# Kernel tuning notes

Hardware: AMD Instinct MI355X
Metric: run time of the kernel (lower is better)

The kernel has to match this reference:

```python
import jax, jax.numpy as jnp
import numpy as np

N_NODES = 10000
N_EDGES = 160000
MUL_N = 64    # node-feature multiplicity per irrep (0e and 1o)
MUL_F = 16    # field-feature multiplicity per irrep
SQ3 = np.sqrt(3.0).astype(np.float32)
SILU_GAIN = np.float32(1.679177)  # e3nn normalize2mom gain for silu


def split_irreps(x, mul):
    # x: [n, mul + 3*mul] laid out e3nn-style: scalars then vectors
    return x[:, :mul], x[:, mul:].reshape(x.shape[0], mul, 3)


def irrep_linear(s, v, Ws, Wv):
    # o3.Linear on (mul x0e + mul x1o): per-irrep channel mixing, 1/sqrt(fan_in)
    inv = np.float32(1.0 / np.sqrt(Ws.shape[0]))
    return (s @ Ws) * inv, jnp.einsum('nui,uv->nvi', v, Wv) * inv


def setup_inputs() -> dict:
    key = jax.random.key(0)
    ks = jax.random.split(key, 30)
    f32 = jnp.float32
    rn = lambda k, sh: jax.random.normal(k, sh, dtype=f32)
    inp = {
        'node_attrs': rn(ks[0], (N_NODES, 10)),
        'node_feats': rn(ks[1], (N_NODES, MUL_N + 3 * MUL_N)),
        'edge_attrs': rn(ks[2], (N_EDGES, 4)),
        'edge_feats': rn(ks[3], (N_EDGES, 8)),
        'field_feats': rn(ks[4], (N_NODES, MUL_F + 3 * MUL_F)),
        'edge_index': jax.random.randint(ks[5], (2, N_EDGES), 0, N_NODES, dtype=jnp.int32),
        # o3.Linear weights (linear1, linear2)
        'W1s': rn(ks[6], (MUL_N, MUL_N)), 'W1v': rn(ks[7], (MUL_N, MUL_N)),
        'W2s': rn(ks[8], (MUL_N, MUL_N)), 'W2v': rn(ks[9], (MUL_N, MUL_N)),
        # FullyConnectedNet [8,64,64,64,256]
        'mlp_w1': rn(ks[10], (8, 64)), 'mlp_w2': rn(ks[11], (64, 64)),
        'mlp_w3': rn(ks[12], (64, 64)), 'mlp_w4': rn(ks[13], (64, 4 * MUL_N)),
        # linear_v_sender / linear_v_receiver: 128x0e+128x1o -> 16x0e+16x1o
        'Wvs_s': rn(ks[14], (2 * MUL_N, MUL_F)), 'Wvs_v': rn(ks[15], (2 * MUL_N, MUL_F)),
        'Wvr_s': rn(ks[16], (2 * MUL_N, MUL_F)), 'Wvr_v': rn(ks[17], (2 * MUL_N, MUL_F)),
        # final FC tensor products (field x field -> 1x0e)
        'Wfs0': rn(ks[18], (MUL_F, MUL_F)), 'Wfs1': rn(ks[19], (MUL_F, MUL_F)),
        'Wfr0': rn(ks[20], (MUL_F, MUL_F)), 'Wfr1': rn(ks[21], (MUL_F, MUL_F)),
        # LinearInFieldChargesBlock FC TP: node x field -> 1x0e+1x1o
        'Wmp_ss': rn(ks[22], (MUL_N, MUL_F)), 'Wmp_vv': rn(ks[23], (MUL_N, MUL_F)),
        'Wmp_sv': rn(ks[24], (MUL_N, MUL_F)), 'Wmp_vs': rn(ks[25], (MUL_N, MUL_F)),
    }
    return inp


def reference(node_attrs, node_feats, edge_attrs, edge_feats, field_feats,
              W1s, W1v, W2s, W2v, mlp_w1, mlp_w2, mlp_w3, mlp_w4,
              Wvs_s, Wvs_v, Wvr_s, Wvr_v, Wfs0, Wfs1, Wfr0, Wfr1,
              Wmp_ss, Wmp_vv, Wmp_sv, Wmp_vs, edge_index):
    sender, receiver = edge_index[0], edge_index[1]
    num_nodes = node_feats.shape[0]

    # conv_tp weight MLP (e3nn FullyConnectedNet)
    h = edge_feats
    for W in (mlp_w1, mlp_w2, mlp_w3):
        h = jax.nn.silu((h @ W) * np.float32(1.0 / np.sqrt(W.shape[0]))) * SILU_GAIN
    tp_w = (h @ mlp_w4) * np.float32(1.0 / np.sqrt(mlp_w4.shape[0]))  # [E, 4*MUL_N]
    w = tp_w.reshape(-1, 4, MUL_N)

    ns, nv = split_irreps(node_feats, MUL_N)
    l1s, l1v = irrep_linear(ns, nv, W1s, W1v)
    l2s, l2v = irrep_linear(ns, nv, W2s, W2v)
    bs = l1s[sender] + l2s[receiver]   # [E, MUL_N]
    bv = l1v[sender] + l2v[receiver]   # [E, MUL_N, 3]

    y0 = edge_attrs[:, 0:1]            # [E,1] 0e harmonic
    y1 = edge_attrs[:, 1:4]            # [E,3] 1o harmonic
    # uvu CG tensor product with per-edge weights
    m00 = w[:, 0] * bs * y0                                          # 0e x 0e -> 0e
    m11 = w[:, 1] * jnp.einsum('eui,ei->eu', bv, y1) / SQ3           # 1o x 1o -> 0e
    m01 = w[:, 2][:, :, None] * bs[:, :, None] * y1[:, None, :]      # 0e x 1o -> 1o
    m10 = w[:, 3][:, :, None] * bv * y0[:, :, None]                  # 1o x 0e -> 1o
    ms = jnp.concatenate([m00, m11], axis=1)    # [E, 128]
    mv = jnp.concatenate([m01, m10], axis=1)    # [E, 128, 3]

    As, Av = irrep_linear(ms, mv, Wvs_s, Wvs_v)
    Bs, Bv = irrep_linear(ms, mv, Wvr_s, Wvr_v)

    fs, fv = split_irreps(field_feats, MUL_F)
    alpha = np.float32(1.0 / np.sqrt(2 * MUL_F * MUL_F))
    p_s = (jnp.einsum('eu,ev,uv->e', As, fs[sender], Wfs0)
           + jnp.einsum('eui,evi,uv->e', Av, fv[sender], Wfs1) / SQ3) * alpha
    p_r = (jnp.einsum('eu,ev,uv->e', Bs, fs[receiver], Wfr0)
           + jnp.einsum('eui,evi,uv->e', Bv, fv[receiver], Wfr1) / SQ3) * alpha
    p_ji = np.float32(0.1) * (p_s + p_r)   # [E]

    charges = (jax.ops.segment_sum(p_ji, receiver, num_segments=num_nodes)
               - jax.ops.segment_sum(p_ji, sender, num_segments=num_nodes))

    # field-dependent multipoles (FC TP, zero_charges=True then charge slot overwritten)
    a2 = np.float32(1.0 / np.sqrt(2 * MUL_N * MUL_F))
    mp0 = (jnp.einsum('nu,nv,uv->n', ns, fs, Wmp_ss)
           + jnp.einsum('nui,nvi,uv->n', nv, fv, Wmp_vv) / SQ3) * a2
    mp1 = (jnp.einsum('nu,nvi,uv->ni', ns, fv, Wmp_sv)
           + jnp.einsum('nui,nv,uv->ni', nv, fs, Wmp_vs)) * a2
    mpoles = np.float32(0.01) * jnp.concatenate([mp0[:, None], mp1], axis=1)  # [N,4]
    mpoles = mpoles.at[:, 0].set(charges)
    return mpoles[:, None, :], p_ji[:, None]
```

## Files before the change

### kernel.cpp

```cpp
#include <hip/hip_runtime.h>

#define NN 10000
#define NE 160000

#define INV8   0.35355339059327373f
#define QINV   0.125f
#define GAIN   1.679177f
#define ISQ3   0.57735026918962576f
#define FINALS 4.8828125e-5f
#define MPSC   2.2097086912079612e-4f

typedef __attribute__((ext_vector_type(8))) short bf16x8;
typedef __attribute__((ext_vector_type(4))) float f32x4;

__device__ __forceinline__ float4 ld4(const float* p){ return *(const float4*)p; }
__device__ __forceinline__ float sil(float x){ return x*GAIN/(1.f+__expf(-x)); }
__device__ __forceinline__ unsigned short f2b(float f){
  unsigned u = __float_as_uint(f);
  return (unsigned short)((u + 0x7FFFu + ((u>>16)&1u)) >> 16);
}
__device__ __forceinline__ float b2f(unsigned short b){
  return __uint_as_float(((unsigned)b) << 16);
}
__device__ __forceinline__ void st4b(unsigned short* p, float a, float b, float c, float d){
  unsigned long long v = (unsigned long long)f2b(a)
                       | ((unsigned long long)f2b(b) << 16)
                       | ((unsigned long long)f2b(c) << 32)
                       | ((unsigned long long)f2b(d) << 48);
  *(unsigned long long*)p = v;
}
__device__ __forceinline__ void up8(const unsigned short* p, float* f){
  const uint4 v = *(const uint4*)p;
  f[0]=__uint_as_float(v.x<<16); f[1]=__uint_as_float(v.x&0xFFFF0000u);
  f[2]=__uint_as_float(v.y<<16); f[3]=__uint_as_float(v.y&0xFFFF0000u);
  f[4]=__uint_as_float(v.z<<16); f[5]=__uint_as_float(v.z&0xFFFF0000u);
  f[6]=__uint_as_float(v.w<<16); f[7]=__uint_as_float(v.w&0xFFFF0000u);
}
#define C4(v,i) (((const float*)&(v))[i])

__global__ __launch_bounds__(256) void sort_zero(unsigned* __restrict__ hist){
  hist[blockIdx.x*256 + threadIdx.x] = 0u;
}
__global__ __launch_bounds__(256) void sort_hist(const int* __restrict__ eidx,
                                                 unsigned* __restrict__ hist){
  const int e = blockIdx.x*256 + threadIdx.x;
  atomicAdd(&hist[eidx[NE + e]], 1u);
}
__global__ __launch_bounds__(256) void sort_scan(const unsigned* __restrict__ hist,
                                                 unsigned* __restrict__ offs){
  __shared__ unsigned part[256];
  __shared__ unsigned base[256];
  const int t = threadIdx.x;
  unsigned s = 0;
  #pragma unroll
  for (int i = 0; i < 40; ++i) s += hist[t*40 + i];
  part[t] = s;
  __syncthreads();
  if (t == 0) {
    unsigned run = 0;
    for (int i = 0; i < 256; ++i) { base[i] = run; run += part[i]; }
  }
  __syncthreads();
  unsigned run = base[t];
  #pragma unroll
  for (int i = 0; i < 40; ++i) { offs[t*40 + i] = run; run += hist[t*40 + i]; }
}
__global__ __launch_bounds__(256) void sort_scatter(const int* __restrict__ eidx,
                                                    unsigned* __restrict__ offs,
                                                    unsigned* __restrict__ sorted){
  const int e = blockIdx.x*256 + threadIdx.x;
  const unsigned pos = atomicAdd(&offs[eidx[NE + e]], 1u);
  sorted[pos] = (unsigned)e;
}
__global__ __launch_bounds__(256) void permute_kernel(
    const unsigned* __restrict__ sorted,
    const float* __restrict__ efe, const float* __restrict__ ea,
    const int* __restrict__ eidx,
    float* __restrict__ pefe, float* __restrict__ pea,
    int* __restrict__ psr, int* __restrict__ peid)
{
  const int i = blockIdx.x*256 + threadIdx.x;
  const int e = (int)sorted[i];
  const float4 a = ld4(efe + (size_t)e*8);
  const float4 b = ld4(efe + (size_t)e*8 + 4);
  *(float4*)(pefe + (size_t)i*8)     = a;
  *(float4*)(pefe + (size_t)i*8 + 4) = b;
  *(float4*)(pea  + (size_t)i*4)     = ld4(ea + (size_t)e*4);
  psr[i]      = eidx[e];
  psr[NE + i] = eidx[NE + e];
  peid[i]     = e;
}

#define WQ_STRIDE 260
__global__ __launch_bounds__(256, 2) void edge_fused_kernel(
    const float* __restrict__ efe,
    const float* __restrict__ mw1, const float* __restrict__ mw2,
    const float* __restrict__ mw3, const float* __restrict__ mw4,
    const float* __restrict__ ea, const int* __restrict__ eidx,
    const int* __restrict__ peid,
    const unsigned short* __restrict__ wsS, const unsigned short* __restrict__ wsR,
    float* __restrict__ out)
{
  __shared__ __align__(16) unsigned char pool[8192 + 128*WQ_STRIDE*2];
  unsigned short* W4q = (unsigned short*)pool;
  unsigned short* W1t = (unsigned short*)(pool + 8192);
  unsigned short* W2t = (unsigned short*)(pool + 12288);
  unsigned short* W3t = (unsigned short*)(pool + 20480);
  unsigned short* H   = (unsigned short*)(pool + 28672);
  unsigned short* WQ  = (unsigned short*)(pool + 8192);

  const int tid = threadIdx.x;
  const int wv  = tid >> 6;
  const int l   = tid & 63;
  const int eb  = blockIdx.x * 128;

  #pragma unroll
  for (int it = 0; it < 16; ++it) {
    const int i = tid + 256*it, e = i >> 5, k = i & 31;
    H[e*64 + (k ^ ((e&7)<<3))] = (k < 8) ? f2b(efe[(size_t)(eb+e)*8 + k]) : 0;
  }
  #pragma unroll
  for (int it = 0; it < 8; ++it) {
    const int i = tid + 256*it, n = i >> 5, k = i & 31;
    W1t[n*32 + (k ^ ((n&3)<<3))] = (k < 8) ? f2b(mw1[k*64 + n]) : 0;
  }
  #pragma unroll
  for (int it = 0; it < 16; ++it) {
    const int i = tid + 256*it, k = i >> 6, n = i & 63;
    W2t[n*64 + (k ^ ((n&7)<<3))] = f2b(mw2[k*64 + n]);
    W3t[n*64 + (k ^ ((n&7)<<3))] = f2b(mw3[k*64 + n]);
  }
  __syncthreads();

  const int arow = l & 15;
  const int koff = (l >> 4) * 8;

  {
    bf16x8 a[8];
    #pragma unroll
    for (int mf = 0; mf < 8; ++mf) {
      const int e = mf*16 + arow;
      a[mf] = *(const bf16x8*)&H[e*64 + (koff ^ ((e&7)<<3))];
    }
    const int n = wv*16 + arow;
    const bf16x8 b = *(const bf16x8*)&W1t[n*32 + (koff ^ ((n&3)<<3))];
    __syncthreads();
    f32x4 acc[8];
    #pragma unroll
    for (int mf = 0; mf < 8; ++mf) {
      acc[mf] = (f32x4){0.f,0.f,0.f,0.f};
      acc[mf] = __builtin_amdgcn_mfma_f32_16x16x32_bf16(a[mf], b, acc[mf], 0, 0, 0);
    }
    #pragma unroll
    for (int mf = 0; mf < 8; ++mf)
      #pragma unroll
      for (int rg = 0; rg < 4; ++rg) {
        const int e = mf*16 + (l>>4)*4 + rg, j = wv*16 + arow;
        H[e*64 + (j ^ ((e&7)<<3))] = f2b(sil(acc[mf][rg]*INV8));
      }
    __syncthreads();
  }

  const unsigned short* Wt[2] = { W2t, W3t };
  #pragma unroll
  for (int ly = 0; ly < 2; ++ly) {
    bf16x8 a[16];
    #pragma unroll
    for (int mf = 0; mf < 8; ++mf)
      #pragma unroll
      for (int ks = 0; ks < 2; ++ks) {
        const int e = mf*16 + arow, kb = ks*32 + koff;
        a[mf*2+ks] = *(const bf16x8*)&H[e*64 + (kb ^ ((e&7)<<3))];
      }
    const int n = wv*16 + arow;
    bf16x8 b0, b1;
    {
      const int kb0 = koff, kb1 = 32 + koff;
      b0 = *(const bf16x8*)&Wt[ly][n*64 + (kb0 ^ ((n&7)<<3))];
      b1 = *(const bf16x8*)&Wt[ly][n*64 + (kb1 ^ ((n&7)<<3))];
    }
    __syncthreads();
    f32x4 acc[8];
    #pragma unroll
    for (int mf = 0; mf < 8; ++mf) {
      acc[mf] = (f32x4){0.f,0.f,0.f,0.f};
      acc[mf] = __builtin_amdgcn_mfma_f32_16x16x32_bf16(a[mf*2+0], b0, acc[mf], 0, 0, 0);
      acc[mf] = __builtin_amdgcn_mfma_f32_16x16x32_bf16(a[mf*2+1], b1, acc[mf], 0, 0, 0);
    }
    #pragma unroll
    for (int mf = 0; mf < 8; ++mf)
      #pragma unroll
      for (int rg = 0; rg < 4; ++rg) {
        const int e = mf*16 + (l>>4)*4 + rg, j = wv*16 + arow;
        H[e*64 + (j ^ ((e&7)<<3))] = f2b(sil(acc[mf][rg]*QINV));
      }
    __syncthreads();
  }

  bf16x8 a4[16];
  #pragma unroll
  for (int mf = 0; mf < 8; ++mf)
    #pragma unroll
    for (int ks = 0; ks < 2; ++ks) {
      const int e = mf*16 + arow, kb = ks*32 + koff;
      a4[mf*2+ks] = *(const bf16x8*)&H[e*64 + (kb ^ ((e&7)<<3))];
    }

  for (int q = 0; q < 4; ++q) {
    #pragma unroll
    for (int it = 0; it < 16; ++it) {
      const int i = tid + 256*it, k = i >> 6, nn = i & 63;
      W4q[nn*64 + (k ^ ((nn&7)<<3))] = f2b(mw4[k*256 + q*64 + nn]);
    }
    __syncthreads();

    const int n = wv*16 + arow;
    const bf16x8 b0 = *(const bf16x8*)&W4q[n*64 + ((koff     ) ^ ((n&7)<<3))];
    const bf16x8 b1 = *(const bf16x8*)&W4q[n*64 + ((32 + koff) ^ ((n&7)<<3))];
    f32x4 acc[8];
    #pragma unroll
    for (int mf = 0; mf < 8; ++mf) {
      acc[mf] = (f32x4){0.f,0.f,0.f,0.f};
      acc[mf] = __builtin_amdgcn_mfma_f32_16x16x32_bf16(a4[mf*2+0], b0, acc[mf], 0, 0, 0);
      acc[mf] = __builtin_amdgcn_mfma_f32_16x16x32_bf16(a4[mf*2+1], b1, acc[mf], 0, 0, 0);
    }
    #pragma unroll
    for (int mf = 0; mf < 8; ++mf)
      #pragma unroll
      for (int rg = 0; rg < 4; ++rg) {
        const int e = mf*16 + (l>>4)*4 + rg;
        const int j = q*64 + wv*16 + arow;
        WQ[e*WQ_STRIDE + j] = f2b(acc[mf][rg]);
      }
    __syncthreads();
  }

  {
    const int el  = tid >> 1;
    const int sub = tid & 1;
    const int e   = eb + el;
    const int s = eidx[e];
    const int r = eidx[NE + e];
    const float4 y = ld4(ea + (size_t)e*4);

    float accS = 0.f, accR = 0.f;
    const unsigned short* Sb = wsS + (size_t)s*768 + sub*384;
    const unsigned short* Rb = wsR + (size_t)r*768 + sub*384;
    const unsigned short* wrow = WQ + el*WQ_STRIDE;
    #pragma unroll 2
    for (int t = 0; t < 8; ++t) {
      const int uq = sub*8 + t;
      const unsigned short* Sr = Sb + t*48;
      const unsigned short* Rr = Rb + t*48;
      float S[48], R[48];
      up8(Sr+ 0, S+ 0); up8(Sr+ 8, S+ 8); up8(Sr+16, S+16);
      up8(Sr+24, S+24); up8(Sr+32, S+32); up8(Sr+40, S+40);
      up8(Rr+ 0, R+ 0); up8(Rr+ 8, R+ 8); up8(Rr+16, R+16);
      up8(Rr+24, R+24); up8(Rr+32, R+32); up8(Rr+40, R+40);

      float wq[16];
      #pragma unroll
      for (int m = 0; m < 4; ++m) {
        const unsigned long long v = *(const unsigned long long*)(wrow + m*64 + uq*4);
        #pragma unroll
        for (int d = 0; d < 4; ++d)
          wq[m*4+d] = b2f((unsigned short)(v >> (16*d)));
      }

      #pragma unroll
      for (int d = 0; d < 4; ++d) {
        const float bs = S[d]    + R[d];
        const float b0 = S[4+d]  + R[4+d];
        const float b1 = S[8+d]  + R[8+d];
        const float b2 = S[12+d] + R[12+d];
        const float bvy = b0*y.y + b1*y.z + b2*y.w;
        const float m0 = wq[d]    * bs * y.x;
        const float m1 = wq[4+d]  * bvy;
        const float m2 = wq[8+d]  * bs;
        const float m3 = wq[12+d] * y.x;
        accS += m0*S[16+d] + m1*S[20+d]
              + m2*(y.y*S[24+d] + y.z*S[28+d] + y.w*S[32+d])
              + m3*(b0*S[36+d] + b1*S[40+d] + b2*S[44+d]);
        accR += m0*R[16+d] + m1*R[20+d]
              + m2*(y.y*R[24+d] + y.z*R[28+d] + y.w*R[32+d])
              + m3*(b0*R[36+d] + b1*R[40+d] + b2*R[44+d]);
      }
    }
    float acc = FINALS * (accS + accR);
    acc += __shfl_xor(acc, 1, 64);
    if (sub == 0) {
      out[NN*4 + peid[e]] = acc;
      atomicAdd(out + (size_t)r*4, acc);
      atomicAdd(out + (size_t)s*4, -acc);
    }
  }
}

__global__ __launch_bounds__(256) void node_kernel(
    const float* __restrict__ nf, const float* __restrict__ ff,
    const float* __restrict__ W1s, const float* __restrict__ W1v,
    const float* __restrict__ W2s, const float* __restrict__ W2v,
    const float* __restrict__ Wvss, const float* __restrict__ Wvsv,
    const float* __restrict__ Wvrs, const float* __restrict__ Wvrv,
    const float* __restrict__ Wfs0, const float* __restrict__ Wfs1,
    const float* __restrict__ Wfr0, const float* __restrict__ Wfr1,
    const float* __restrict__ Wmsv, const float* __restrict__ Wmvs,
    unsigned short* __restrict__ wsS, unsigned short* __restrict__ wsR,
    float* __restrict__ out)
{
  const int lane = threadIdx.x & 63;
  const int Wid  = blockIdx.x * 4 + (threadIdx.x >> 6);
  const int p    = __builtin_amdgcn_readfirstlane(Wid & 7);
  const int grp  = __builtin_amdgcn_readfirstlane(Wid >> 3);
  const int n = grp * 64 + lane;
  if (n >= NN) return;
  const float* nrow = nf + (size_t)n * 256;
  const int vb = p * 8;
  const size_t rec = (size_t)n * 768;

  float a1s[8], a2s[8], a1v[3][8], a2v[3][8], t1[16];
  #pragma unroll
  for (int j = 0; j < 8; ++j){ a1s[j]=0.f; a2s[j]=0.f;
    a1v[0][j]=0.f; a1v[1][j]=0.f; a1v[2][j]=0.f;
    a2v[0][j]=0.f; a2v[1][j]=0.f; a2v[2][j]=0.f; }
  #pragma unroll
  for (int j = 0; j < 16; ++j) t1[j]=0.f;

  for (int u = 0; u < 64; ++u) {
    const float su  = nrow[u];
    const float nv0 = nrow[64+u*3+0];
    const float nv1 = nrow[64+u*3+1];
    const float nv2 = nrow[64+u*3+2];
    const float4 s1a = ld4(W1s+u*64+vb), s1b = ld4(W1s+u*64+vb+4);
    const float4 s2a = ld4(W2s+u*64+vb), s2b = ld4(W2s+u*64+vb+4);
    const float4 v1a = ld4(W1v+u*64+vb), v1b = ld4(W1v+u*64+vb+4);
    const float4 v2a = ld4(W2v+u*64+vb), v2b = ld4(W2v+u*64+vb+4);
    #pragma unroll
    for (int d = 0; d < 4; ++d) {
      a1s[d]     += su*C4(s1a,d);  a1s[4+d]     += su*C4(s1b,d);
      a2s[d]     += su*C4(s2a,d);  a2s[4+d]     += su*C4(s2b,d);
      a1v[0][d]  += nv0*C4(v1a,d); a1v[0][4+d]  += nv0*C4(v1b,d);
      a1v[1][d]  += nv1*C4(v1a,d); a1v[1][4+d]  += nv1*C4(v1b,d);
      a1v[2][d]  += nv2*C4(v1a,d); a1v[2][4+d]  += nv2*C4(v1b,d);
      a2v[0][d]  += nv0*C4(v2a,d); a2v[0][4+d]  += nv0*C4(v2b,d);
      a2v[1][d]  += nv1*C4(v2a,d); a2v[1][4+d]  += nv1*C4(v2b,d);
      a2v[2][d]  += nv2*C4(v2a,d); a2v[2][4+d]  += nv2*C4(v2b,d);
    }
    if (p == 0) {
      #pragma unroll
      for (int q = 0; q < 4; ++q) {
        const float4 m = ld4(Wmsv + u*16 + q*4);
        t1[q*4]   += su*m.x; t1[q*4+1] += su*m.y;
        t1[q*4+2] += su*m.z; t1[q*4+3] += su*m.w;
      }
    }
  }
  #pragma unroll
  for (int hh = 0; hh < 2; ++hh) {
    const int uq = 2*p + hh, o = hh*4;
    unsigned short* S = wsS + rec + uq*48;
    unsigned short* R = wsR + rec + uq*48;
    st4b(S+0,  a1s[o]*QINV, a1s[o+1]*QINV, a1s[o+2]*QINV, a1s[o+3]*QINV);
    st4b(S+4,  a1v[0][o]*QINV, a1v[0][o+1]*QINV, a1v[0][o+2]*QINV, a1v[0][o+3]*QINV);
    st4b(S+8,  a1v[1][o]*QINV, a1v[1][o+1]*QINV, a1v[1][o+2]*QINV, a1v[1][o+3]*QINV);
    st4b(S+12, a1v[2][o]*QINV, a1v[2][o+1]*QINV, a1v[2][o+2]*QINV, a1v[2][o+3]*QINV);
    st4b(R+0,  a2s[o]*QINV, a2s[o+1]*QINV, a2s[o+2]*QINV, a2s[o+3]*QINV);
    st4b(R+4,  a2v[0][o]*QINV, a2v[0][o+1]*QINV, a2v[0][o+2]*QINV, a2v[0][o+3]*QINV);
    st4b(R+8,  a2v[1][o]*QINV, a2v[1][o+1]*QINV, a2v[1][o+2]*QINV, a2v[1][o+3]*QINV);
    st4b(R+12, a2v[2][o]*QINV, a2v[2][o+1]*QINV, a2v[2][o+2]*QINV, a2v[2][o+3]*QINV);
  }

  float fsv[16], fvv[48];
  {
    const float* fr = ff + (size_t)n*64;
    #pragma unroll
    for (int q = 0; q < 4; ++q) {
      const float4 t = ld4(fr + q*4);
      fsv[q*4]=t.x; fsv[q*4+1]=t.y; fsv[q*4+2]=t.z; fsv[q*4+3]=t.w;
    }
    #pragma unroll
    for (int q = 0; q < 12; ++q) {
      const float4 t = ld4(fr + 16 + q*4);
      fvv[q*4]=t.x; fvv[q*4+1]=t.y; fvv[q*4+2]=t.z; fvv[q*4+3]=t.w;
    }
  }

  if (p == 0) {
    float m0=0.f, m1=0.f, m2=0.f;
    #pragma unroll
    for (int v = 0; v < 16; ++v) {
      m0 += t1[v]*fvv[v*3]; m1 += t1[v]*fvv[v*3+1]; m2 += t1[v]*fvv[v*3+2];
    }
    for (int u = 0; u < 64; ++u) {
      float t2 = 0.f;
      #pragma unroll
      for (int q = 0; q < 4; ++q) {
        const float4 w = ld4(Wmvs + u*16 + q*4);
        t2 += w.x*fsv[q*4] + w.y*fsv[q*4+1] + w.z*fsv[q*4+2] + w.w*fsv[q*4+3];
      }
      m0 += nrow[64+u*3+0]*t2;
      m1 += nrow[64+u*3+1]*t2;
      m2 += nrow[64+u*3+2]*t2;
    }
    float* o = out + (size_t)n*4;
    o[0] = 0.f;
    o[1] = MPSC*m0; o[2] = MPSC*m1; o[3] = MPSC*m2;
  }

  float gsA[16], gsB[16], gvA[48], gvB[48];
  #pragma unroll
  for (int up = 0; up < 16; ++up) {
    float sA=0.f,sB=0.f,vA0=0.f,vA1=0.f,vA2=0.f,vB0=0.f,vB1=0.f,vB2=0.f;
    #pragma unroll
    for (int q = 0; q < 4; ++q) {
      const float4 w0 = ld4(Wfs0 + up*16 + q*4);
      const float4 w1 = ld4(Wfs1 + up*16 + q*4);
      const float4 w2 = ld4(Wfr0 + up*16 + q*4);
      const float4 w3 = ld4(Wfr1 + up*16 + q*4);
      #pragma unroll
      for (int d = 0; d < 4; ++d) {
        const int v = q*4+d;
        sA  += C4(w0,d)*fsv[v];
        sB  += C4(w2,d)*fsv[v];
        vA0 += C4(w1,d)*fvv[v*3]; vA1 += C4(w1,d)*fvv[v*3+1]; vA2 += C4(w1,d)*fvv[v*3+2];
        vB0 += C4(w3,d)*fvv[v*3]; vB1 += C4(w3,d)*fvv[v*3+1]; vB2 += C4(w3,d)*fvv[v*3+2];
      }
    }
    gsA[up]=sA; gsB[up]=sB;
    gvA[up*3]=vA0; gvA[up*3+1]=vA1; gvA[up*3+2]=vA2;
    gvB[up*3]=vB0; gvB[up*3+1]=vB1; gvB[up*3+2]=vB2;
  }

  #pragma unroll
  for (int tq = 0; tq < 4; ++tq) {
    float qa[4], qb[4], ra[3][4], rb[3][4];
    #pragma unroll
    for (int d = 0; d < 4; ++d) {
      const int U = p*16 + tq*4 + d;
      float aq=0.f,bq=0.f,a0=0.f,a1=0.f,a2=0.f,b0=0.f,b1=0.f,b2=0.f;
      #pragma unroll
      for (int q = 0; q < 4; ++q) {
        const float4 ws_ = ld4(Wvss + U*16 + q*4);
        const float4 wr_ = ld4(Wvrs + U*16 + q*4);
        const float4 wv_ = ld4(Wvsv + U*16 + q*4);
        const float4 wu_ = ld4(Wvrv + U*16 + q*4);
        #pragma unroll
        for (int dd = 0; dd < 4; ++dd) {
          const int up = q*4+dd;
          aq += C4(ws_,dd)*gsA[up];
          bq += C4(wr_,dd)*gsB[up];
          a0 += C4(wv_,dd)*gvA[up*3]; a1 += C4(wv_,dd)*gvA[up*3+1]; a2 += C4(wv_,dd)*gvA[up*3+2];
          b0 += C4(wu_,dd)*gvB[up*3]; b1 += C4(wu_,dd)*gvB[up*3+1]; b2 += C4(wu_,dd)*gvB[up*3+2];
        }
      }
      qa[d]=aq; qb[d]=bq;
      ra[0][d]=a0*ISQ3; ra[1][d]=a1*ISQ3; ra[2][d]=a2*ISQ3;
      rb[0][d]=b0*ISQ3; rb[1][d]=b1*ISQ3; rb[2][d]=b2*ISQ3;
    }
    if (p < 4) {
      const int uq = p*4 + tq;
      unsigned short* S = wsS + rec + uq*48;
      unsigned short* R = wsR + rec + uq*48;
      st4b(S+16, qa[0],qa[1],qa[2],qa[3]);
      st4b(S+24, ra[0][0],ra[0][1],ra[0][2],ra[0][3]);
      st4b(S+28, ra[1][0],ra[1][1],ra[1][2],ra[1][3]);
      st4b(S+32, ra[2][0],ra[2][1],ra[2][2],ra[2][3]);
      st4b(R+16, qb[0],qb[1],qb[2],qb[3]);
      st4b(R+24, rb[0][0],rb[0][1],rb[0][2],rb[0][3]);
      st4b(R+28, rb[1][0],rb[1][1],rb[1][2],rb[1][3]);
      st4b(R+32, rb[2][0],rb[2][1],rb[2][2],rb[2][3]);
    } else {
      const int uq = (p-4)*4 + tq;
      unsigned short* S = wsS + rec + uq*48;
      unsigned short* R = wsR + rec + uq*48;
      st4b(S+20, qa[0]*ISQ3,qa[1]*ISQ3,qa[2]*ISQ3,qa[3]*ISQ3);
      st4b(S+36, ra[0][0],ra[0][1],ra[0][2],ra[0][3]);
      st4b(S+40, ra[1][0],ra[1][1],ra[1][2],ra[1][3]);
      st4b(S+44, ra[2][0],ra[2][1],ra[2][2],ra[2][3]);
      st4b(R+20, qb[0]*ISQ3,qb[1]*ISQ3,qb[2]*ISQ3,qb[3]*ISQ3);
      st4b(R+36, rb[0][0],rb[0][1],rb[0][2],rb[0][3]);
      st4b(R+40, rb[1][0],rb[1][1],rb[1][2],rb[1][3]);
      st4b(R+44, rb[2][0],rb[2][1],rb[2][2],rb[2][3]);
    }
  }
}

extern "C" void kernel_launch(void* const* d_in, const int* in_sizes, int n_in,
                              void* d_out, int out_size, void* d_ws, size_t ws_size,
                              hipStream_t stream) {
  (void)in_sizes; (void)n_in; (void)out_size; (void)ws_size;
  const float* node_feats  = (const float*)d_in[1];
  const float* edge_attrs  = (const float*)d_in[2];
  const float* edge_feats  = (const float*)d_in[3];
  const float* field_feats = (const float*)d_in[4];
  const int*   edge_index  = (const int*)  d_in[5];
  const float* W1s  = (const float*)d_in[6];
  const float* W1v  = (const float*)d_in[7];
  const float* W2s  = (const float*)d_in[8];
  const float* W2v  = (const float*)d_in[9];
  const float* mw1  = (const float*)d_in[10];
  const float* mw2  = (const float*)d_in[11];
  const float* mw3  = (const float*)d_in[12];
  const float* mw4  = (const float*)d_in[13];
  const float* Wvss = (const float*)d_in[14];
  const float* Wvsv = (const float*)d_in[15];
  const float* Wvrs = (const float*)d_in[16];
  const float* Wvrv = (const float*)d_in[17];
  const float* Wfs0 = (const float*)d_in[18];
  const float* Wfs1 = (const float*)d_in[19];
  const float* Wfr0 = (const float*)d_in[20];
  const float* Wfr1 = (const float*)d_in[21];
  const float* Wmsv = (const float*)d_in[24];
  const float* Wmvs = (const float*)d_in[25];

  float* out = (float*)d_out;
  unsigned short* wsS = (unsigned short*)d_ws;
  unsigned short* wsR = wsS + (size_t)NN*768;
  float* pefe   = (float*)(wsR + (size_t)NN*768);
  float* pea    = pefe + (size_t)NE*8;
  int*   psr    = (int*)(pea + (size_t)NE*4);
  int*   peid   = psr + (size_t)2*NE;
  unsigned* hist   = (unsigned*)(peid + NE);
  unsigned* offs   = hist + 10240;
  unsigned* sorted = offs + 10240;

  hipLaunchKernelGGL(sort_zero,    dim3(40),  dim3(256), 0, stream, hist);
  hipLaunchKernelGGL(sort_hist,    dim3(625), dim3(256), 0, stream, edge_index, hist);
  hipLaunchKernelGGL(sort_scan,    dim3(1),   dim3(256), 0, stream, hist, offs);
  hipLaunchKernelGGL(sort_scatter, dim3(625), dim3(256), 0, stream, edge_index, offs, sorted);
  hipLaunchKernelGGL(permute_kernel, dim3(625), dim3(256), 0, stream,
      sorted, edge_feats, edge_attrs, edge_index, pefe, pea, psr, peid);

  hipLaunchKernelGGL(node_kernel, dim3(314), dim3(256), 0, stream,
      node_feats, field_feats, W1s, W1v, W2s, W2v, Wvss, Wvsv, Wvrs, Wvrv,
      Wfs0, Wfs1, Wfr0, Wfr1, Wmsv, Wmvs, wsS, wsR, out);
  hipLaunchKernelGGL(edge_fused_kernel, dim3(NE/128), dim3(256), 0, stream,
      pefe, mw1, mw2, mw3, mw4, pea, psr, peid, wsS, wsR, out);
}
```

Baseline: 231.4 us.

## Fuse edge scatter with permute, parallelize scan, replace zero kernel with memset

The counting-sort scatter and the edge permutation become one kernel, so the intermediate sorted-index array is no longer written and re-read and one launch disappears. The single-block scan swaps its serial thread-0 prefix loop for wave shuffle scans plus a small cross-wave sum, and caches histogram values in registers instead of reading them twice. The histogram zeroing kernel is replaced by hipMemsetAsync. The fused kernel now writes to scattered positions, which is less coalesced than the old writes that followed sorted order.

Measured after the change: 227.7 us. Within noise of the previous version (-1.6%).

```diff
diff --git a/kernel.cpp b/kernel.cpp
--- a/kernel.cpp
+++ b/kernel.cpp
@@ -38,9 +38,6 @@
 }
 #define C4(v,i) (((const float*)&(v))[i])
 
-__global__ __launch_bounds__(256) void sort_zero(unsigned* __restrict__ hist){
-  hist[blockIdx.x*256 + threadIdx.x] = 0u;
-}
 __global__ __launch_bounds__(256) void sort_hist(const int* __restrict__ eidx,
                                                  unsigned* __restrict__ hist){
   const int e = blockIdx.x*256 + threadIdx.x;
@@ -48,47 +45,46 @@
 }
 __global__ __launch_bounds__(256) void sort_scan(const unsigned* __restrict__ hist,
                                                  unsigned* __restrict__ offs){
-  __shared__ unsigned part[256];
-  __shared__ unsigned base[256];
+  __shared__ unsigned wsum[4];
   const int t = threadIdx.x;
+  const int lane = t & 63, w = t >> 6;
+  unsigned local[40];
   unsigned s = 0;
   #pragma unroll
-  for (int i = 0; i < 40; ++i) s += hist[t*40 + i];
-  part[t] = s;
+  for (int i = 0; i < 40; ++i) { local[i] = hist[t*40 + i]; s += local[i]; }
+  unsigned inc = s;
+  #pragma unroll
+  for (int off = 1; off < 64; off <<= 1) {
+    const unsigned n = __shfl_up(inc, off, 64);
+    if (lane >= off) inc += n;
+  }
+  if (lane == 63) wsum[w] = inc;
   __syncthreads();
-  if (t == 0) {
-    unsigned run = 0;
-    for (int i = 0; i < 256; ++i) { base[i] = run; run += part[i]; }
-  }
-  __syncthreads();
-  unsigned run = base[t];
-  #pragma unroll
-  for (int i = 0; i < 40; ++i) { offs[t*40 + i] = run; run += hist[t*40 + i]; }
-}
-__global__ __launch_bounds__(256) void sort_scatter(const int* __restrict__ eidx,
-                                                    unsigned* __restrict__ offs,
-                                                    unsigned* __restrict__ sorted){
-  const int e = blockIdx.x*256 + threadIdx.x;
-  const unsigned pos = atomicAdd(&offs[eidx[NE + e]], 1u);
-  sorted[pos] = (unsigned)e;
-}
-__global__ __launch_bounds__(256) void permute_kernel(
-    const unsigned* __restrict__ sorted,
+  unsigned base = 0;
+  #pragma unroll
+  for (int i = 0; i < 4; ++i) if (i < w) base += wsum[i];
+  unsigned run = base + inc - s;
+  #pragma unroll
+  for (int i = 0; i < 40; ++i) { offs[t*40 + i] = run; run += local[i]; }
+}
+__global__ __launch_bounds__(256) void sort_scatter_permute(
+    const int* __restrict__ eidx,
     const float* __restrict__ efe, const float* __restrict__ ea,
-    const int* __restrict__ eidx,
+    unsigned* __restrict__ offs,
     float* __restrict__ pefe, float* __restrict__ pea,
     int* __restrict__ psr, int* __restrict__ peid)
 {
-  const int i = blockIdx.x*256 + threadIdx.x;
-  const int e = (int)sorted[i];
+  const int e = blockIdx.x*256 + threadIdx.x;
+  const int r = eidx[NE + e];
+  const unsigned pos = atomicAdd(&offs[r], 1u);
   const float4 a = ld4(efe + (size_t)e*8);
   const float4 b = ld4(efe + (size_t)e*8 + 4);
-  *(float4*)(pefe + (size_t)i*8)     = a;
-  *(float4*)(pefe + (size_t)i*8 + 4) = b;
-  *(float4*)(pea  + (size_t)i*4)     = ld4(ea + (size_t)e*4);
-  psr[i]      = eidx[e];
-  psr[NE + i] = eidx[NE + e];
-  peid[i]     = e;
+  *(float4*)(pefe + (size_t)pos*8)     = a;
+  *(float4*)(pefe + (size_t)pos*8 + 4) = b;
+  *(float4*)(pea  + (size_t)pos*4)     = ld4(ea + (size_t)e*4);
+  psr[pos]      = eidx[e];
+  psr[NE + pos] = r;
+  peid[pos]     = e;
 }
 
 #define WQ_STRIDE 260
@@ -522,14 +518,12 @@
   int*   peid   = psr + (size_t)2*NE;
   unsigned* hist   = (unsigned*)(peid + NE);
   unsigned* offs   = hist + 10240;
-  unsigned* sorted = offs + 10240;
-
-  hipLaunchKernelGGL(sort_zero,    dim3(40),  dim3(256), 0, stream, hist);
-  hipLaunchKernelGGL(sort_hist,    dim3(625), dim3(256), 0, stream, edge_index, hist);
-  hipLaunchKernelGGL(sort_scan,    dim3(1),   dim3(256), 0, stream, hist, offs);
-  hipLaunchKernelGGL(sort_scatter, dim3(625), dim3(256), 0, stream, edge_index, offs, sorted);
-  hipLaunchKernelGGL(permute_kernel, dim3(625), dim3(256), 0, stream,
-      sorted, edge_feats, edge_attrs, edge_index, pefe, pea, psr, peid);
+
+  hipMemsetAsync(hist, 0, 10240*sizeof(unsigned), stream);
+  hipLaunchKernelGGL(sort_hist, dim3(625), dim3(256), 0, stream, edge_index, hist);
+  hipLaunchKernelGGL(sort_scan, dim3(1),   dim3(256), 0, stream, hist, offs);
+  hipLaunchKernelGGL(sort_scatter_permute, dim3(625), dim3(256), 0, stream,
+      edge_index, edge_feats, edge_attrs, offs, pefe, pea, psr, peid);
 
   hipLaunchKernelGGL(node_kernel, dim3(314), dim3(256), 0, stream,
       node_feats, field_feats, W1s, W1v, W2s, W2v, Wvss, Wvsv, Wvrs, Wvrv,
```
